# Kernel tuning notes

Hardware: AMD Instinct MI355X
Metric: run time of the kernel (lower is better)

## Reference

```python
import jax, jax.numpy as jnp
import numpy as np

B, C_IN, H, W = 4, 256, 64, 64
LATENT = 256


def conv1x1(x, w, b):
    # x: [B, Cin, H, W], w: [Cout, Cin], b: [Cout]
    return jnp.einsum('bchw,oc->bohw', x, w) + b[None, :, None, None]


def setup_inputs() -> dict:
    key = jax.random.key(0)
    ks = jax.random.split(key, 9)
    s_in = 1.0 / np.sqrt(C_IN)
    s_lat = 1.0 / np.sqrt(LATENT)
    return {
        'x': jax.random.normal(ks[0], (B, C_IN, H, W), dtype=jnp.float32),
        'Wq': jax.random.normal(ks[1], (LATENT, C_IN), dtype=jnp.float32) * s_in,
        'bq': jax.random.normal(ks[2], (LATENT,), dtype=jnp.float32) * 0.01,
        'Wk': jax.random.normal(ks[3], (LATENT, C_IN), dtype=jnp.float32) * s_in,
        'bk': jax.random.normal(ks[4], (LATENT,), dtype=jnp.float32) * 0.01,
        'Wv': jax.random.normal(ks[5], (LATENT, C_IN), dtype=jnp.float32) * s_in,
        'bv': jax.random.normal(ks[6], (LATENT,), dtype=jnp.float32) * 0.01,
        'Wo': jax.random.normal(ks[7], (C_IN, LATENT), dtype=jnp.float32) * s_lat,
        'bo': jax.random.normal(ks[8], (C_IN,), dtype=jnp.float32) * 0.01,
    }


def reference(x, Wq, bq, Wk, bk, Wv, bv, Wo, bo):
    b, _, h, w = x.shape
    n = h * w
    q = conv1x1(x, Wq, bq).reshape(b, LATENT, n)  # [B, L, N]
    k = conv1x1(x, Wk, bk).reshape(b, LATENT, n)
    v = conv1x1(x, Wv, bv).reshape(b, LATENT, n)
    scale = jnp.sqrt(jnp.asarray(LATENT, dtype=x.dtype))
    # attention[b, i, j] = sum_c q[b, c, i] * k[b, c, j]
    attn = jnp.einsum('bci,bcj->bij', q, k) / scale
    # faithful to original: softmax over dim=1 (query index i, per column j)
    attn = jax.nn.softmax(attn, axis=1)
    # res[b, c, j] = sum_i v[b, c, i] * attn[b, i, j]
    res = jnp.einsum('bci,bij->bcj', v, attn).reshape(b, LATENT, h, w)
    return conv1x1(res, Wo, bo)
```

## Files before the change

### kernel.cpp

```cpp
#include <hip/hip_runtime.h>

#define B_  4
#define C_  256
#define N_  4096
#define SCALE 0.0625f

typedef short s8v __attribute__((ext_vector_type(8)));
typedef float f4v __attribute__((ext_vector_type(4)));

static __device__ __forceinline__ ushort f2bf(float f) {
  union { float f; uint u; } v; v.f = f;
  return (ushort)((v.u + 0x7FFFu + ((v.u >> 16) & 1u)) >> 16);
}

__global__ __launch_bounds__(256) void xpose_cast(
    const float* __restrict__ x, ushort* __restrict__ x_t,
    float* __restrict__ den)
{
  const int b  = blockIdx.z;
  const int c0 = blockIdx.y * 64;
  const int n0 = blockIdx.x * 64;
  __shared__ float t[64][65];

  if (blockIdx.y == 0 && threadIdx.x < 64)
    den[b * N_ + n0 + threadIdx.x] = 0.f;

  const int tc = threadIdx.x >> 4;
  const int tn = (threadIdx.x & 15) * 4;
  #pragma unroll
  for (int cc = 0; cc < 64; cc += 16) {
    float4 v = *(const float4*)(x + (size_t)(b * C_ + c0 + cc + tc) * N_ + n0 + tn);
    t[cc + tc][tn + 0] = v.x;
    t[cc + tc][tn + 1] = v.y;
    t[cc + tc][tn + 2] = v.z;
    t[cc + tc][tn + 3] = v.w;
  }
  __syncthreads();

  const int on = threadIdx.x >> 2;
  const int oc = (threadIdx.x & 3) * 16;
  union { ushort us[16]; uint4 q[2]; } o;
  #pragma unroll
  for (int i = 0; i < 16; ++i) o.us[i] = f2bf(t[oc + i][on]);
  ushort* dst = x_t + (size_t)(b * N_ + n0 + on) * C_ + c0 + oc;
  *(uint4*)dst       = o.q[0];
  *(uint4*)(dst + 8) = o.q[1];
}

__global__ __launch_bounds__(256, 2) void qkv_mfma(
    const ushort* __restrict__ x_t,
    const float* __restrict__ Wq, const float* __restrict__ bq,
    const float* __restrict__ Wk, const float* __restrict__ bk,
    const float* __restrict__ Wv, const float* __restrict__ bv,
    ushort* __restrict__ q_t, ushort* __restrict__ k_t, ushort* __restrict__ v_bf)
{
  const int p = blockIdx.z >> 2;
  const int b = blockIdx.z & 3;
  const float* W  = (p == 0) ? Wq : (p == 1) ? Wk : Wv;
  const float* bi = (p == 0) ? bq : (p == 1) ? bk : bv;
  const int l0    = blockIdx.y * 64;
  const int nseg  = blockIdx.x * 512;

  const int tid  = threadIdx.x;
  const int lane = tid & 63;
  const int wave = tid >> 6;
  const int l16  = lane & 15;
  const int quad = lane >> 4;

  __shared__ __align__(16) ushort w_lds[64 * 264];
  __shared__ __align__(16) ushort x_lds[64 * 264];

  for (int g = tid; g < 4096; g += 256) {
    int row = g >> 6, col4 = (g & 63) * 4;
    float4 wv = *(const float4*)(W + (size_t)(l0 + row) * 256 + col4);
    *(ushort4*)&w_lds[row * 264 + col4] =
        make_ushort4(f2bf(wv.x), f2bf(wv.y), f2bf(wv.z), f2bf(wv.w));
  }
  __syncthreads();

  s8v kw[4][8];
  #pragma unroll
  for (int lt = 0; lt < 4; ++lt)
    #pragma unroll
    for (int cs = 0; cs < 8; ++cs)
      kw[lt][cs] = *(const s8v*)&w_lds[(lt * 16 + l16) * 264 + quad * 8 + cs * 32];

  float bias_l[4];
  #pragma unroll
  for (int lt = 0; lt < 4; ++lt) bias_l[lt] = bi[l0 + lt * 16 + l16];

  for (int it = 0; it < 8; ++it) {
    const int n0 = nseg + it * 64;
    {
      const ushort* xseg = x_t + (size_t)(b * N_ + n0) * C_;
      #pragma unroll
      for (int k = 0; k < 8; ++k) {
        int c = tid + k * 256;
        uint4 d = *(const uint4*)(xseg + (size_t)c * 8);
        *(uint4*)&x_lds[(c >> 5) * 264 + (c & 31) * 8] = d;
      }
    }
    __syncthreads();

    f4v s[4];
    #pragma unroll
    for (int lt = 0; lt < 4; ++lt) s[lt] = (f4v){0.f, 0.f, 0.f, 0.f};
    const ushort* xa_base = x_lds + (wave * 16 + l16) * 264 + quad * 8;
    #pragma unroll
    for (int cs = 0; cs < 8; ++cs) {
      s8v xa = *(const s8v*)(xa_base + cs * 32);
      #pragma unroll
      for (int lt = 0; lt < 4; ++lt)
        s[lt] = __builtin_amdgcn_mfma_f32_16x16x32_bf16(xa, kw[lt][cs], s[lt], 0, 0, 0);
    }

    const int nb = n0 + wave * 16 + quad * 4;
    if (p < 2) {
      ushort* outp = (p == 0) ? q_t : k_t;
      #pragma unroll
      for (int lt = 0; lt < 4; ++lt) {
        const int l = l0 + lt * 16 + l16;
        #pragma unroll
        for (int r = 0; r < 4; ++r)
          outp[(size_t)(b * N_ + nb + r) * C_ + l] = f2bf(s[lt][r] + bias_l[lt]);
      }
    } else {
      #pragma unroll
      for (int lt = 0; lt < 4; ++lt) {
        const int c_out = l0 + lt * 16 + l16;
        *(ushort4*)&v_bf[(size_t)(b * C_ + c_out) * N_ + nb] =
            make_ushort4(f2bf(s[lt][0] + bias_l[lt]), f2bf(s[lt][1] + bias_l[lt]),
                         f2bf(s[lt][2] + bias_l[lt]), f2bf(s[lt][3] + bias_l[lt]));
      }
    }
    __syncthreads();
  }
}

__global__ __launch_bounds__(256, 2) void flash8b(
    const ushort* __restrict__ q_t, const ushort* __restrict__ k_t,
    const ushort* __restrict__ v_bf, ushort* __restrict__ res0,
    ushort* __restrict__ res1, float* __restrict__ den)
{
  const int tid  = threadIdx.x;
  const int lane = tid & 63;
  const int wave = tid >> 6;
  const int l16  = lane & 15;
  const int quad = lane >> 4;
  const int jw    = blockIdx.x * 64;
  const int seg   = blockIdx.y;
  const int ibase = seg * 2048;
  const int b     = blockIdx.z;

  const int wqk_j = wave & 1;
  const int wqk_i = wave >> 1;

  __shared__ __align__(16) ushort q_lds[64 * 264];
  __shared__ __align__(16) ushort p_lds[64 * 72];

  s8v kf[2][8];
  #pragma unroll
  for (int jt = 0; jt < 2; ++jt) {
    const ushort* kp = k_t + (size_t)(b * N_ + jw + wqk_j * 32 + jt * 16 + l16) * C_ + quad * 8;
    #pragma unroll
    for (int cs = 0; cs < 8; ++cs) kf[jt][cs] = *(const s8v*)(kp + cs * 32);
  }

  f4v acc[4][4];
  #pragma unroll
  for (int m = 0; m < 4; ++m)
    #pragma unroll
    for (int t = 0; t < 4; ++t) acc[m][t] = (f4v){0.f, 0.f, 0.f, 0.f};
  float dacc0 = 0.f, dacc1 = 0.f;

  const ushort* vbase0 = v_bf + (size_t)(b * C_ + wave * 64 + l16) * N_ + quad * 8;

  for (int it = 0; it < 32; ++it) {
    const int i0 = ibase + it * 64;

    {
      const ushort* qseg = q_t + ((size_t)(b * N_) + i0) * C_;
      #pragma unroll
      for (int k = 0; k < 8; ++k) {
        int c = tid + k * 256;
        uint4 d = *(const uint4*)(qseg + (size_t)c * 8);
        *(uint4*)&q_lds[(c >> 5) * 264 + (c & 31) * 8] = d;
      }
    }

    s8v av[4][2];
    #pragma unroll
    for (int m = 0; m < 4; ++m)
      #pragma unroll
      for (int ks = 0; ks < 2; ++ks)
        av[m][ks] = *(const s8v*)(vbase0 + (size_t)(m * 16) * N_ + i0 + ks * 32);

    __syncthreads();

    #pragma unroll
    for (int itile = 0; itile < 2; ++itile) {
      const int i_loc = (wqk_i * 2 + itile) * 16;
      f4v s0 = (f4v){0.f, 0.f, 0.f, 0.f};
      f4v s1 = (f4v){0.f, 0.f, 0.f, 0.f};
      const ushort* qa_base = q_lds + (i_loc + l16) * 264 + quad * 8;
      #pragma unroll
      for (int cs = 0; cs < 8; ++cs) {
        s8v qa = *(const s8v*)(qa_base + cs * 32);
        s0 = __builtin_amdgcn_mfma_f32_16x16x32_bf16(qa, kf[0][cs], s0, 0, 0, 0);
        s1 = __builtin_amdgcn_mfma_f32_16x16x32_bf16(qa, kf[1][cs], s1, 0, 0, 0);
      }
      {
        float e0 = __expf(s0[0] * SCALE), e1 = __expf(s0[1] * SCALE);
        float e2 = __expf(s0[2] * SCALE), e3 = __expf(s0[3] * SCALE);
        dacc0 += (e0 + e1) + (e2 + e3);
        *(ushort4*)&p_lds[(wqk_j * 32 + l16) * 72 + i_loc + quad * 4] =
            make_ushort4(f2bf(e0), f2bf(e1), f2bf(e2), f2bf(e3));
      }
      {
        float e0 = __expf(s1[0] * SCALE), e1 = __expf(s1[1] * SCALE);
        float e2 = __expf(s1[2] * SCALE), e3 = __expf(s1[3] * SCALE);
        dacc1 += (e0 + e1) + (e2 + e3);
        *(ushort4*)&p_lds[(wqk_j * 32 + 16 + l16) * 72 + i_loc + quad * 4] =
            make_ushort4(f2bf(e0), f2bf(e1), f2bf(e2), f2bf(e3));
      }
    }

    __syncthreads();

    #pragma unroll
    for (int ks = 0; ks < 2; ++ks) {
      s8v pb[4];
      #pragma unroll
      for (int t = 0; t < 4; ++t)
        pb[t] = *(const s8v*)&p_lds[(t * 16 + l16) * 72 + ks * 32 + quad * 8];
      #pragma unroll
      for (int m = 0; m < 4; ++m)
        #pragma unroll
        for (int t = 0; t < 4; ++t)
          acc[m][t] = __builtin_amdgcn_mfma_f32_16x16x32_bf16(av[m][ks], pb[t], acc[m][t], 0, 0, 0);
    }
  }

  dacc0 += __shfl_xor(dacc0, 16);  dacc0 += __shfl_xor(dacc0, 32);
  dacc1 += __shfl_xor(dacc1, 16);  dacc1 += __shfl_xor(dacc1, 32);
  if (lane < 16) {
    atomicAdd(&den[b * N_ + jw + wqk_j * 32 + lane], dacc0);
    atomicAdd(&den[b * N_ + jw + wqk_j * 32 + 16 + lane], dacc1);
  }

  #pragma unroll
  for (int m = 0; m < 4; ++m) {
    const int c0 = wave * 64 + m * 16 + quad * 4;
    #pragma unroll
    for (int t = 0; t < 4; ++t) {
      *(ushort4*)&q_lds[(t * 16 + l16) * 264 + c0] =
          make_ushort4(f2bf(acc[m][t][0]), f2bf(acc[m][t][1]),
                       f2bf(acc[m][t][2]), f2bf(acc[m][t][3]));
    }
  }
  __syncthreads();
  {
    ushort* rp = (seg ? res1 : res0) + (size_t)(b * N_ + jw) * C_;
    #pragma unroll
    for (int k = 0; k < 8; ++k) {
      int c = tid + k * 256;
      int row = c >> 5, col = (c & 31) * 8;
      uint4 d = *(const uint4*)&q_lds[row * 264 + col];
      *(uint4*)&rp[(size_t)row * C_ + col] = d;
    }
  }
}

__global__ __launch_bounds__(256, 2) void out_mfma(
    const ushort* __restrict__ res0, const ushort* __restrict__ res1,
    const float* __restrict__ Wo, const float* __restrict__ bo,
    const float* __restrict__ den, float* __restrict__ out)
{
  const int b    = blockIdx.z;
  const int co0  = blockIdx.y * 64;
  const int nseg = blockIdx.x * 256;

  const int tid  = threadIdx.x;
  const int lane = tid & 63;
  const int wave = tid >> 6;
  const int l16  = lane & 15;
  const int quad = lane >> 4;

  __shared__ __align__(16) ushort w_lds[64 * 264];
  __shared__ __align__(16) ushort r_lds[2][64 * 264];

  for (int g = tid; g < 4096; g += 256) {
    int row = g >> 6, col4 = (g & 63) * 4;
    float4 wv = *(const float4*)(Wo + (size_t)(co0 + row) * 256 + col4);
    *(ushort4*)&w_lds[row * 264 + col4] =
        make_ushort4(f2bf(wv.x), f2bf(wv.y), f2bf(wv.z), f2bf(wv.w));
  }
  __syncthreads();

  s8v kw[4][8];
  #pragma unroll
  for (int lt = 0; lt < 4; ++lt)
    #pragma unroll
    for (int cs = 0; cs < 8; ++cs)
      kw[lt][cs] = *(const s8v*)&w_lds[(lt * 16 + l16) * 264 + quad * 8 + cs * 32];

  float bias_l[4];
  #pragma unroll
  for (int lt = 0; lt < 4; ++lt) bias_l[lt] = bo[co0 + lt * 16 + l16];

  for (int it = 0; it < 4; ++it) {
    const int n0 = nseg + it * 64;
    {
      const ushort* r0 = res0 + (size_t)(b * N_ + n0) * C_;
      const ushort* r1 = res1 + (size_t)(b * N_ + n0) * C_;
      #pragma unroll
      for (int k = 0; k < 8; ++k) {
        int c = tid + k * 256;
        uint4 d0 = *(const uint4*)(r0 + (size_t)c * 8);
        uint4 d1 = *(const uint4*)(r1 + (size_t)c * 8);
        *(uint4*)&r_lds[0][(c >> 5) * 264 + (c & 31) * 8] = d0;
        *(uint4*)&r_lds[1][(c >> 5) * 264 + (c & 31) * 8] = d1;
      }
    }
    __syncthreads();

    f4v s[4];
    #pragma unroll
    for (int lt = 0; lt < 4; ++lt) s[lt] = (f4v){0.f, 0.f, 0.f, 0.f};
    #pragma unroll
    for (int buf = 0; buf < 2; ++buf) {
      const ushort* ra_base = r_lds[buf] + (wave * 16 + l16) * 264 + quad * 8;
      #pragma unroll
      for (int cs = 0; cs < 8; ++cs) {
        s8v ra = *(const s8v*)(ra_base + cs * 32);
        #pragma unroll
        for (int lt = 0; lt < 4; ++lt)
          s[lt] = __builtin_amdgcn_mfma_f32_16x16x32_bf16(ra, kw[lt][cs], s[lt], 0, 0, 0);
      }
    }

    const int nb = n0 + wave * 16 + quad * 4;
    float4 dv = *(const float4*)(den + (size_t)b * N_ + nb);
    const float di0 = 1.0f / dv.x, di1 = 1.0f / dv.y, di2 = 1.0f / dv.z, di3 = 1.0f / dv.w;
    #pragma unroll
    for (int lt = 0; lt < 4; ++lt) {
      const int co = co0 + lt * 16 + l16;
      *(float4*)&out[(size_t)(b * C_ + co) * N_ + nb] =
          make_float4(s[lt][0] * di0 + bias_l[lt], s[lt][1] * di1 + bias_l[lt],
                      s[lt][2] * di2 + bias_l[lt], s[lt][3] * di3 + bias_l[lt]);
    }
    __syncthreads();
  }
}

extern "C" void kernel_launch(void* const* d_in, const int* in_sizes, int n_in,
                              void* d_out, int out_size, void* d_ws, size_t ws_size,
                              hipStream_t stream)
{
  const float* x  = (const float*)d_in[0];
  const float* Wq = (const float*)d_in[1];
  const float* bq = (const float*)d_in[2];
  const float* Wk = (const float*)d_in[3];
  const float* bk = (const float*)d_in[4];
  const float* Wv = (const float*)d_in[5];
  const float* bv = (const float*)d_in[6];
  const float* Wo = (const float*)d_in[7];
  const float* bo = (const float*)d_in[8];
  float* out = (float*)d_out;

  char* ws = (char*)d_ws;
  ushort* q_t  = (ushort*)(ws);
  ushort* k_t  = (ushort*)(ws + (size_t)8  * 1024 * 1024);
  ushort* v_bf = (ushort*)(ws + (size_t)16 * 1024 * 1024);
  ushort* res0 = (ushort*)(ws + (size_t)24 * 1024 * 1024);
  ushort* res1 = (ushort*)(ws + (size_t)32 * 1024 * 1024);
  float*  den  = (float*) (ws + (size_t)40 * 1024 * 1024);
  ushort* x_t  = (ushort*)(ws + (size_t)40 * 1024 * 1024 + 65536);

  xpose_cast<<<dim3(64, 4, 4), dim3(256), 0, stream>>>(x, x_t, den);
  qkv_mfma <<<dim3(8, 4, 12),  dim3(256), 0, stream>>>(x_t, Wq, bq, Wk, bk, Wv, bv, q_t, k_t, v_bf);
  flash8b  <<<dim3(64, 2, 4),  dim3(256), 0, stream>>>(q_t, k_t, v_bf, res0, res1, den);
  out_mfma <<<dim3(16, 4, 4),  dim3(256), 0, stream>>>(res0, res1, Wo, bo, den, out);
}
```

Measured before the change: 206.9 us.

## Load Q tile via global_load_lds with XOR-swizzled LDS layouts and MFMA priority

```diff
diff --git a/kernel.cpp b/kernel.cpp
--- a/kernel.cpp
+++ b/kernel.cpp
@@ -11,6 +11,12 @@
 static __device__ __forceinline__ ushort f2bf(float f) {
   union { float f; uint u; } v; v.f = f;
   return (ushort)((v.u + 0x7FFFu + ((v.u >> 16) & 1u)) >> 16);
+}
+
+static __device__ __forceinline__ void gload_lds16(const ushort* g, ushort* l) {
+  __builtin_amdgcn_global_load_lds(
+      (const __attribute__((address_space(1))) void*)g,
+      (__attribute__((address_space(3))) void*)l, 16, 0, 0);
 }
 
 __global__ __launch_bounds__(256) void xpose_cast(
@@ -155,8 +161,8 @@
   const int wqk_j = wave & 1;
   const int wqk_i = wave >> 1;
 
-  __shared__ __align__(16) ushort q_lds[64 * 264];
-  __shared__ __align__(16) ushort p_lds[64 * 72];
+  __shared__ __align__(16) ushort q_lds[64 * 256];
+  __shared__ __align__(16) ushort p_lds[64 * 64];
 
   s8v kf[2][8];
   #pragma unroll
@@ -180,11 +186,12 @@
 
     {
       const ushort* qseg = q_t + ((size_t)(b * N_) + i0) * C_;
+      const int plo = lane & 31;
       #pragma unroll
       for (int k = 0; k < 8; ++k) {
-        int c = tid + k * 256;
-        uint4 d = *(const uint4*)(qseg + (size_t)c * 8);
-        *(uint4*)&q_lds[(c >> 5) * 264 + (c & 31) * 8] = d;
+        const int row = k * 8 + wave * 2 + (lane >> 5);
+        const ushort* src = qseg + row * 256 + ((plo ^ (row & 7)) << 3);
+        gload_lds16(src, &q_lds[k * 2048 + wave * 512]);
       }
     }
 
@@ -202,25 +209,33 @@
       const int i_loc = (wqk_i * 2 + itile) * 16;
       f4v s0 = (f4v){0.f, 0.f, 0.f, 0.f};
       f4v s1 = (f4v){0.f, 0.f, 0.f, 0.f};
-      const ushort* qa_base = q_lds + (i_loc + l16) * 264 + quad * 8;
+      const int qrow = i_loc + l16;
+      const ushort* qa_row = q_lds + qrow * 256;
+      const int qsw = qrow & 7;
+      __builtin_amdgcn_s_setprio(1);
       #pragma unroll
       for (int cs = 0; cs < 8; ++cs) {
-        s8v qa = *(const s8v*)(qa_base + cs * 32);
+        s8v qa = *(const s8v*)(qa_row + (((quad + 4 * cs) ^ qsw) << 3));
         s0 = __builtin_amdgcn_mfma_f32_16x16x32_bf16(qa, kf[0][cs], s0, 0, 0, 0);
         s1 = __builtin_amdgcn_mfma_f32_16x16x32_bf16(qa, kf[1][cs], s1, 0, 0, 0);
       }
+      __builtin_amdgcn_s_setprio(0);
       {
         float e0 = __expf(s0[0] * SCALE), e1 = __expf(s0[1] * SCALE);
         float e2 = __expf(s0[2] * SCALE), e3 = __expf(s0[3] * SCALE);
         dacc0 += (e0 + e1) + (e2 + e3);
-        *(ushort4*)&p_lds[(wqk_j * 32 + l16) * 72 + i_loc + quad * 4] =
+        const int row = wqk_j * 32 + l16;
+        const int col = i_loc + quad * 4;
+        *(ushort4*)&p_lds[row * 64 + ((((col >> 3) ^ (row & 7)) << 3) | (col & 7))] =
             make_ushort4(f2bf(e0), f2bf(e1), f2bf(e2), f2bf(e3));
       }
       {
         float e0 = __expf(s1[0] * SCALE), e1 = __expf(s1[1] * SCALE);
         float e2 = __expf(s1[2] * SCALE), e3 = __expf(s1[3] * SCALE);
         dacc1 += (e0 + e1) + (e2 + e3);
-        *(ushort4*)&p_lds[(wqk_j * 32 + 16 + l16) * 72 + i_loc + quad * 4] =
+        const int row = wqk_j * 32 + 16 + l16;
+        const int col = i_loc + quad * 4;
+        *(ushort4*)&p_lds[row * 64 + ((((col >> 3) ^ (row & 7)) << 3) | (col & 7))] =
             make_ushort4(f2bf(e0), f2bf(e1), f2bf(e2), f2bf(e3));
       }
     }
@@ -231,13 +246,18 @@
     for (int ks = 0; ks < 2; ++ks) {
       s8v pb[4];
       #pragma unroll
-      for (int t = 0; t < 4; ++t)
-        pb[t] = *(const s8v*)&p_lds[(t * 16 + l16) * 72 + ks * 32 + quad * 8];
+      for (int t = 0; t < 4; ++t) {
+        const int row = t * 16 + l16;
+        const int col = ks * 32 + quad * 8;
+        pb[t] = *(const s8v*)&p_lds[row * 64 + (((col >> 3) ^ (row & 7)) << 3)];
+      }
+      __builtin_amdgcn_s_setprio(1);
       #pragma unroll
       for (int m = 0; m < 4; ++m)
         #pragma unroll
         for (int t = 0; t < 4; ++t)
           acc[m][t] = __builtin_amdgcn_mfma_f32_16x16x32_bf16(av[m][ks], pb[t], acc[m][t], 0, 0, 0);
+      __builtin_amdgcn_s_setprio(0);
     }
   }
 
@@ -253,7 +273,8 @@
     const int c0 = wave * 64 + m * 16 + quad * 4;
     #pragma unroll
     for (int t = 0; t < 4; ++t) {
-      *(ushort4*)&q_lds[(t * 16 + l16) * 264 + c0] =
+      const int row = t * 16 + l16;
+      *(ushort4*)&q_lds[row * 256 + ((((c0 >> 3) ^ (row & 7)) << 3) | (c0 & 7))] =
           make_ushort4(f2bf(acc[m][t][0]), f2bf(acc[m][t][1]),
                        f2bf(acc[m][t][2]), f2bf(acc[m][t][3]));
     }
@@ -264,9 +285,9 @@
     #pragma unroll
     for (int k = 0; k < 8; ++k) {
       int c = tid + k * 256;
-      int row = c >> 5, col = (c & 31) * 8;
-      uint4 d = *(const uint4*)&q_lds[row * 264 + col];
-      *(uint4*)&rp[(size_t)row * C_ + col] = d;
+      int row = c >> 5, ch = c & 31;
+      uint4 d = *(const uint4*)&q_lds[row * 256 + ((ch ^ (row & 7)) << 3)];
+      *(uint4*)&rp[(size_t)row * C_ + ch * 8] = d;
     }
   }
 }
```

Result: no change. 208.1 us (+0.6%).
